# Performance work log

Measured on AMD Instinct MI355X. Metric: run time of the kernel, lower is better.

Reference implementation:

```python
import jax, jax.numpy as jnp
import numpy as np

B, L, H, E, MODES = 32, 2048, 8, 64, 64
SCALE = 1.0 / (512 * 512)  # 1/(in_channels*out_channels)


def setup_inputs() -> dict:
    key = jax.random.key(0)
    kq, kk, kv, kwr, kwi = jax.random.split(key, 5)
    # frequency mode selection: shuffled range(L//2), first MODES, sorted (get_frequency_modes)
    rng = np.random.default_rng(0)
    index = np.sort(rng.permutation(L // 2)[:MODES]).astype(np.int32)
    return {
        "q": jax.random.normal(kq, (B, L, H, E), dtype=jnp.float32),
        "k": jax.random.normal(kk, (B, L, H, E), dtype=jnp.float32),
        "v": jax.random.normal(kv, (B, L, H, E), dtype=jnp.float32),
        "w_real": SCALE * jax.random.uniform(kwr, (H, E, E, MODES), dtype=jnp.float32),
        "w_imag": SCALE * jax.random.uniform(kwi, (H, E, E, MODES), dtype=jnp.float32),
        "index": jnp.asarray(index),
    }


def reference(q, k, v, w_real, w_imag, index):
    # q: [B, L, H, E]; k, v unused by FourierBlock
    Bq, Lq, Hq, Eq = q.shape
    x = jnp.transpose(q, (0, 2, 3, 1))            # [B, H, E, L]
    x_ft = jnp.fft.rfft(x, axis=-1)               # [B, H, E, L//2+1] complex
    xs = jnp.take(x_ft, index, axis=-1)           # gather selected modes: [B, H, E, M]
    W = w_real + 1j * w_imag                      # [H, E, E, M] complex
    # vectorized per-mode complex einsum ('bhi,hio->bho' over all modes m)
    out = jnp.einsum('bhim,hiom->bhom', xs, W)    # [B, H, E, M]
    n_freq = Lq // 2 + 1
    # original writes mode wi into slot wi (0..M-1), rest stay zero
    out_ft = jnp.concatenate(
        [out, jnp.zeros((Bq, Hq, Eq, n_freq - out.shape[-1]), dtype=out.dtype)], axis=-1)
    return jnp.fft.irfft(out_ft, n=Lq, axis=-1)   # [B, H, E, L] real
```

## Files before the change

### kernel.cpp

```cpp
#include <hip/hip_runtime.h>
#include <math.h>

#define NB 32
#define NL 2048
#define NH 8
#define NE 64
#define NM 64
#define MRI 128
#define BK 128
#define NCH 16

typedef __attribute__((ext_vector_type(8))) __bf16 bf16x8;
typedef __attribute__((ext_vector_type(2))) __bf16 bf16x2;
typedef __attribute__((ext_vector_type(8))) unsigned short us8;
typedef __attribute__((ext_vector_type(4))) unsigned short us4;
typedef __attribute__((ext_vector_type(4))) float f32x4;
typedef __attribute__((ext_vector_type(16))) float f32x16;

__device__ __forceinline__ unsigned short f2bf(float x) {
  unsigned int u = __builtin_bit_cast(unsigned int, x);
  u = (u + 0x7fffu + ((u >> 16) & 1u)) >> 16;
  return (unsigned short)u;
}
__device__ __forceinline__ float bf2f(unsigned short u) {
  return __builtin_bit_cast(float, (unsigned int)u << 16);
}
__device__ __forceinline__ unsigned int pk2(float lo, float hi) {
  bf16x2 v;
  v[0] = (__bf16)lo;
  v[1] = (__bf16)hi;
  return __builtin_bit_cast(unsigned int, v);
}

__global__ void tables_k(const int* __restrict__ idx,
                         const float* __restrict__ wr, const float* __restrict__ wi,
                         unsigned short* __restrict__ Tf, unsigned short* __restrict__ IT,
                         unsigned short* __restrict__ WBr, unsigned short* __restrict__ WBi) {
  int gid = blockIdx.x * blockDim.x + threadIdx.x;
  const float w0 = 6.283185307179586f / (float)NL;
  {
    int j = gid & 7, lane_ = (gid >> 3) & 63, tm_ = (gid >> 9) & 3;
    int ks_ = (gid >> 11) & 3, kh_ = (gid >> 13) & 1, c_ = gid >> 14;
    int row = tm_ * 32 + (lane_ & 31);
    int m = row & 63;
    int k = c_ * 128 + kh_ * 64 + ks_ * 16 + (lane_ >> 5) * 8 + j;
    int f = idx[m];
    float s, c2;
    sincosf((float)((f * k) & (NL - 1)) * w0, &s, &c2);
    Tf[gid] = f2bf(row < 64 ? c2 : -s);
  }
  {
    int lp = gid >> 7, k = gid & 127;
    int m = k & 63;
    float s, c;
    sincosf((float)((m * lp) & (NL - 1)) * w0, &s, &c);
    float v = (k < 64) ? ((m == 0 ? 1.0f : 2.0f) / (float)NL) * c
                       : (m == 0 ? 0.0f : (-2.0f / (float)NL) * s);
    IT[gid] = f2bf(v);
  }
  {
    const float2* wr2 = (const float2*)wr;
    const float2* wi2 = (const float2*)wi;
    unsigned int* obr = (unsigned int*)WBr;
    unsigned int* obi = (unsigned int*)WBi;
#pragma unroll
    for (int r = 0; r < 4; ++r) {
      int j = r * 262144 + gid;
      float2 a = wr2[j];
      float2 b2 = wi2[j];
      obr[j] = pk2(a.x, a.y);
      obi[j] = pk2(b2.x, b2.y);
    }
  }
}

__global__ __launch_bounds__(1024) void fused_k(const float* __restrict__ q,
                                                const unsigned short* __restrict__ T,
                                                const unsigned short* __restrict__ IT,
                                                const unsigned short* __restrict__ WBr,
                                                const unsigned short* __restrict__ WBi,
                                                float* __restrict__ out) {
  __shared__ __align__(16) char smem[85504];
  int t = threadIdx.x, lane = t & 63, wid = t >> 6;
  int h = blockIdx.x & 7, b = blockIdx.x >> 3;

  {
    char* bC = smem + 34816;
    char* bN = smem + 34816 + 16896;
    char* bX = smem + 34816 + 33792;
    const float* qb = q + ((size_t)b * NL * NH + h) * NE;
    int tm = wid & 3;
    int te = (wid >> 2) & 1;
    int kh = wid >> 3;
    int eq = t & 15, lq = t >> 4;
    f32x16 acc32 = {};
    f32x4 qA[2], qB[2];
    us8 arA[4], arB[4];

    auto qload = [&](int c, f32x4* qr) {
#pragma unroll
      for (int p = 0; p < 2; ++p)
        qr[p] = *(const f32x4*)(qb + (size_t)(c * BK + lq * 2 + p) * (NH * NE) + eq * 4);
    };
    auto writesB = [&](const f32x4* qr, char* bb) {
#pragma unroll
      for (int j = 0; j < 4; ++j) {
        int e = eq * 4 + j;
        *(unsigned int*)(bb + e * 264 + lq * 4) = pk2(qr[0][j], qr[1][j]);
      }
    };
    auto loadA = [&](int c, us8* ar) {
#pragma unroll
      for (int ks = 0; ks < 4; ++ks)
        ar[ks] = *(const us8*)(T + ((((size_t)c * 2 + kh) * 4 + ks) * 4 + tm) * 512 + lane * 8);
    };
    auto compute = [&](const us8* ar, const char* bb) {
#pragma unroll
      for (int ks = 0; ks < 4; ++ks) {
        int k0 = (kh * 4 + ks) * 16;
        int e = te * 32 + (lane & 31);
        int boff = e * 264 + (k0 + (lane >> 5) * 8) * 2;
        uint2 blo = *(const uint2*)(bb + boff);
        uint2 bhi = *(const uint2*)(bb + boff + 8);
        bf16x8 bfr = __builtin_bit_cast(bf16x8, make_uint4(blo.x, blo.y, bhi.x, bhi.y));
        acc32 = __builtin_amdgcn_mfma_f32_32x32x16_bf16(
            __builtin_bit_cast(bf16x8, ar[ks]), bfr, acc32, 0, 0, 0);
      }
    };
    auto rot = [&]() {
      char* tmp = bC;
      bC = bN;
      bN = bX;
      bX = tmp;
    };

    qload(0, qA);
    qload(1, qB);
    loadA(0, arA);
    writesB(qA, bC);
    asm volatile("s_waitcnt lgkmcnt(0)" ::: "memory");
    __builtin_amdgcn_s_barrier();
    for (int c = 0; c < NCH; c += 2) {
      loadA(c + 1, arB);
      if (c + 2 < NCH) qload(c + 2, qA);
      __builtin_amdgcn_sched_barrier(0);
      compute(arA, bC);
      writesB(qB, bN);
      asm volatile("s_waitcnt lgkmcnt(0)" ::: "memory");
      __builtin_amdgcn_s_barrier();
      rot();
      if (c + 2 < NCH) loadA(c + 2, arA);
      if (c + 3 < NCH) qload(c + 3, qB);
      __builtin_amdgcn_sched_barrier(0);
      compute(arB, bC);
      if (c + 2 < NCH) {
        writesB(qA, bN);
        asm volatile("s_waitcnt lgkmcnt(0)" ::: "memory");
        __builtin_amdgcn_s_barrier();
      }
      rot();
    }
    __syncthreads();

    float* scr = (float*)(smem + 34816);
    int tile = wid & 7;
    if (kh == 1) {
#pragma unroll
      for (int r = 0; r < 16; ++r) {
        int row = (r & 3) + 8 * (r >> 2) + 4 * (lane >> 5);
        scr[tile * 1024 + row * 32 + (lane & 31)] = acc32[r];
      }
    }
    __syncthreads();
    if (kh == 0) {
#pragma unroll
      for (int r = 0; r < 16; ++r) {
        int row = (r & 3) + 8 * (r >> 2) + 4 * (lane >> 5);
        float v = acc32[r] + scr[tile * 1024 + row * 32 + (lane & 31)];
        int grow = tm * 32 + row;
        int gcol = te * 32 + (lane & 31);
        int off = (grow * 272 + gcol * 4) ^ (((grow >> 3) & 7) << 4);
        *(float*)(smem + off) = v;
      }
    }
  }
  __syncthreads();

  {
    char* OtB = smem + 67584;
    int o = t >> 4, mq = t & 15;
    const unsigned short* wbr = WBr + (size_t)h * 262144 + o * 64 + mq * 4;
    const unsigned short* wbi = WBi + (size_t)h * 262144 + o * 64 + mq * 4;
    float orr[4] = {}, oii[4] = {};
#pragma unroll 2
    for (int ib = 0; ib < 16; ++ib) {
      f32x4 xr4[4], xi4[4];
#pragma unroll
      for (int mi = 0; mi < 4; ++mi) {
        int m = mq * 4 + mi;
        xr4[mi] = *(const f32x4*)(smem + ((m * 272 + ib * 16) ^ (((m >> 3) & 7) << 4)));
        xi4[mi] = *(const f32x4*)(smem + (((64 + m) * 272 + ib * 16) ^ (((m >> 3) & 7) << 4)));
      }
      us4 wr4[4], wi4[4];
#pragma unroll
      for (int ii = 0; ii < 4; ++ii) {
        int i = ib * 4 + ii;
        wr4[ii] = *(const us4*)(wbr + (size_t)i * 4096);
        wi4[ii] = *(const us4*)(wbi + (size_t)i * 4096);
      }
#pragma unroll
      for (int ii = 0; ii < 4; ++ii)
#pragma unroll
        for (int mi = 0; mi < 4; ++mi) {
          float wrv = bf2f(wr4[ii][mi]);
          float wiv = bf2f(wi4[ii][mi]);
          orr[mi] += xr4[mi][ii] * wrv - xi4[mi][ii] * wiv;
          oii[mi] += xr4[mi][ii] * wiv + xi4[mi][ii] * wrv;
        }
    }
    uint2 vr = make_uint2(pk2(orr[0], orr[1]), pk2(orr[2], orr[3]));
    uint2 vi = make_uint2(pk2(oii[0], oii[1]), pk2(oii[2], oii[3]));
    *(uint2*)(OtB + ((o * 256 + mq * 8) ^ ((o & 7) << 4))) = vr;
    *(uint2*)(OtB + ((o * 256 + 128 + mq * 8) ^ ((o & 7) << 4))) = vi;
  }
  __syncthreads();

  {
    const char* OtB = smem + 67584;
    bf16x8 af[2][8];
#pragma unroll
    for (int rg2 = 0; rg2 < 2; ++rg2)
#pragma unroll
      for (int ks = 0; ks < 8; ++ks) {
        int row = rg2 * 32 + (lane & 31);
        int off = (row * 256 + ks * 32 + (lane >> 5) * 16) ^ ((row & 7) << 4);
        af[rg2][ks] = __builtin_bit_cast(bf16x8, *(const us8*)(OtB + off));
      }
    float* ob = out + ((size_t)(b * 8 + h) * 64) * NL;
    int l0 = wid * 128;
    for (int ct = 0; ct < 4; ++ct) {
      int lr = l0 + ct * 32 + (lane & 31);
      f32x16 a2[2] = {};
#pragma unroll
      for (int ks = 0; ks < 8; ++ks) {
        bf16x8 bv = __builtin_bit_cast(
            bf16x8, *(const us8*)(IT + (size_t)lr * MRI + ks * 16 + (lane >> 5) * 8));
        a2[0] = __builtin_amdgcn_mfma_f32_32x32x16_bf16(af[0][ks], bv, a2[0], 0, 0, 0);
        a2[1] = __builtin_amdgcn_mfma_f32_32x32x16_bf16(af[1][ks], bv, a2[1], 0, 0, 0);
      }
#pragma unroll
      for (int rg2 = 0; rg2 < 2; ++rg2)
#pragma unroll
        for (int rg = 0; rg < 16; ++rg) {
          int row = rg2 * 32 + ((rg & 3) + 8 * (rg >> 2) + 4 * (lane >> 5));
          __builtin_nontemporal_store(a2[rg2][rg], &ob[(size_t)row * NL + lr]);
        }
    }
  }
}

extern "C" void kernel_launch(void* const* d_in, const int* in_sizes, int n_in,
                              void* d_out, int out_size, void* d_ws, size_t ws_size,
                              hipStream_t stream) {
  const float* q = (const float*)d_in[0];
  const float* wr = (const float*)d_in[3];
  const float* wi = (const float*)d_in[4];
  const int* idx = (const int*)d_in[5];
  float* out = (float*)d_out;
  char* ws = (char*)d_ws;

  constexpr size_t TBYTES = (size_t)MRI * NL * 2;
  constexpr size_t WBBYTES = (size_t)NH * NE * NE * NM * 2;
  constexpr size_t NEED = 2 * TBYTES + 2 * WBBYTES;
  if (ws_size < NEED) return;

  unsigned short* Tf = (unsigned short*)ws;
  unsigned short* IT = (unsigned short*)(ws + TBYTES);
  unsigned short* WBr = (unsigned short*)(ws + 2 * TBYTES);
  unsigned short* WBi = (unsigned short*)(ws + 2 * TBYTES + WBBYTES);

  hipLaunchKernelGGL(tables_k, dim3(1024), dim3(256), 0, stream, idx, wr, wi, Tf, IT, WBr, WBi);
  hipLaunchKernelGGL(fused_k, dim3(NB * NH), dim3(1024), 0, stream, q, Tf, IT, WBr, WBi, out);
}
```

Measured before the change: 82.61 us.

## Halve fused kernel block to 512 threads, drop split-K reduction and shrink LDS

The fused kernel now runs 512 threads per block instead of 1024, so each wave covers the full K range of the forward DFT GEMM. This removes the split-K halves and their shared-memory reduction step. Per-thread work doubles in every stage: more q loads, more A fragments, 8 modes per thread in the complex mix, and 256 L-columns per wave in the inverse transform. Shared memory falls from about 85KB to 52KB, with a launch bound hint of 4 blocks. The gains are fewer barriers and more co-resident blocks, at the cost of higher register pressure and less parallelism inside each block.

```diff
diff --git a/kernel.cpp b/kernel.cpp
--- a/kernel.cpp
+++ b/kernel.cpp
@@ -13,7 +13,6 @@
 typedef __attribute__((ext_vector_type(8))) __bf16 bf16x8;
 typedef __attribute__((ext_vector_type(2))) __bf16 bf16x2;
 typedef __attribute__((ext_vector_type(8))) unsigned short us8;
-typedef __attribute__((ext_vector_type(4))) unsigned short us4;
 typedef __attribute__((ext_vector_type(4))) float f32x4;
 typedef __attribute__((ext_vector_type(16))) float f32x16;
 
@@ -74,57 +73,57 @@
   }
 }
 
-__global__ __launch_bounds__(1024) void fused_k(const float* __restrict__ q,
-                                                const unsigned short* __restrict__ T,
-                                                const unsigned short* __restrict__ IT,
-                                                const unsigned short* __restrict__ WBr,
-                                                const unsigned short* __restrict__ WBi,
-                                                float* __restrict__ out) {
-  __shared__ __align__(16) char smem[85504];
+__global__ __launch_bounds__(512, 4) void fused_k(const float* __restrict__ q,
+                                                  const unsigned short* __restrict__ T,
+                                                  const unsigned short* __restrict__ IT,
+                                                  const unsigned short* __restrict__ WBr,
+                                                  const unsigned short* __restrict__ WBi,
+                                                  float* __restrict__ out) {
+  __shared__ __align__(16) char smem[53248];
   int t = threadIdx.x, lane = t & 63, wid = t >> 6;
   int h = blockIdx.x & 7, b = blockIdx.x >> 3;
 
   {
-    char* bC = smem + 34816;
-    char* bN = smem + 34816 + 16896;
-    char* bX = smem + 34816 + 33792;
+    char* bC = smem;
+    char* bN = smem + 16896;
+    char* bX = smem + 33792;
     const float* qb = q + ((size_t)b * NL * NH + h) * NE;
     int tm = wid & 3;
-    int te = (wid >> 2) & 1;
-    int kh = wid >> 3;
+    int te = wid >> 2;
     int eq = t & 15, lq = t >> 4;
     f32x16 acc32 = {};
-    f32x4 qA[2], qB[2];
-    us8 arA[4], arB[4];
+    f32x4 qA[4], qB[4];
+    us8 arA[8], arB[8];
 
     auto qload = [&](int c, f32x4* qr) {
 #pragma unroll
-      for (int p = 0; p < 2; ++p)
-        qr[p] = *(const f32x4*)(qb + (size_t)(c * BK + lq * 2 + p) * (NH * NE) + eq * 4);
+      for (int p = 0; p < 4; ++p)
+        qr[p] = *(const f32x4*)(qb + (size_t)(c * BK + lq * 4 + p) * (NH * NE) + eq * 4);
     };
     auto writesB = [&](const f32x4* qr, char* bb) {
 #pragma unroll
       for (int j = 0; j < 4; ++j) {
         int e = eq * 4 + j;
-        *(unsigned int*)(bb + e * 264 + lq * 4) = pk2(qr[0][j], qr[1][j]);
+        *(uint2*)(bb + e * 264 + lq * 8) =
+            make_uint2(pk2(qr[0][j], qr[1][j]), pk2(qr[2][j], qr[3][j]));
       }
     };
     auto loadA = [&](int c, us8* ar) {
 #pragma unroll
-      for (int ks = 0; ks < 4; ++ks)
-        ar[ks] = *(const us8*)(T + ((((size_t)c * 2 + kh) * 4 + ks) * 4 + tm) * 512 + lane * 8);
+      for (int kf = 0; kf < 8; ++kf)
+        ar[kf] = *(const us8*)(
+            T + ((((size_t)c * 2 + (kf >> 2)) * 4 + (kf & 3)) * 4 + tm) * 512 + lane * 8);
     };
     auto compute = [&](const us8* ar, const char* bb) {
 #pragma unroll
-      for (int ks = 0; ks < 4; ++ks) {
-        int k0 = (kh * 4 + ks) * 16;
+      for (int kf = 0; kf < 8; ++kf) {
         int e = te * 32 + (lane & 31);
-        int boff = e * 264 + (k0 + (lane >> 5) * 8) * 2;
+        int boff = e * 264 + (kf * 16 + (lane >> 5) * 8) * 2;
         uint2 blo = *(const uint2*)(bb + boff);
         uint2 bhi = *(const uint2*)(bb + boff + 8);
         bf16x8 bfr = __builtin_bit_cast(bf16x8, make_uint4(blo.x, blo.y, bhi.x, bhi.y));
         acc32 = __builtin_amdgcn_mfma_f32_32x32x16_bf16(
-            __builtin_bit_cast(bf16x8, ar[ks]), bfr, acc32, 0, 0, 0);
+            __builtin_bit_cast(bf16x8, ar[kf]), bfr, acc32, 0, 0, 0);
       }
     };
     auto rot = [&]() {
@@ -162,71 +161,60 @@
     }
     __syncthreads();
 
-    float* scr = (float*)(smem + 34816);
-    int tile = wid & 7;
-    if (kh == 1) {
-#pragma unroll
-      for (int r = 0; r < 16; ++r) {
-        int row = (r & 3) + 8 * (r >> 2) + 4 * (lane >> 5);
-        scr[tile * 1024 + row * 32 + (lane & 31)] = acc32[r];
-      }
-    }
-    __syncthreads();
-    if (kh == 0) {
-#pragma unroll
-      for (int r = 0; r < 16; ++r) {
-        int row = (r & 3) + 8 * (r >> 2) + 4 * (lane >> 5);
-        float v = acc32[r] + scr[tile * 1024 + row * 32 + (lane & 31)];
-        int grow = tm * 32 + row;
-        int gcol = te * 32 + (lane & 31);
-        int off = (grow * 272 + gcol * 4) ^ (((grow >> 3) & 7) << 4);
-        *(float*)(smem + off) = v;
-      }
+#pragma unroll
+    for (int rg = 0; rg < 16; ++rg) {
+      int row = (rg & 3) + 8 * (rg >> 2) + 4 * (lane >> 5);
+      int grow = tm * 32 + row;
+      int gcol = te * 32 + (lane & 31);
+      int off = (grow * 272 + gcol * 4) ^ (((grow >> 3) & 7) << 4);
+      *(float*)(smem + off) = acc32[rg];
     }
   }
   __syncthreads();
 
   {
-    char* OtB = smem + 67584;
-    int o = t >> 4, mq = t & 15;
-    const unsigned short* wbr = WBr + (size_t)h * 262144 + o * 64 + mq * 4;
-    const unsigned short* wbi = WBi + (size_t)h * 262144 + o * 64 + mq * 4;
-    float orr[4] = {}, oii[4] = {};
-#pragma unroll 2
+    char* OtB = smem + 36864;
+    int o = t >> 3, mq = t & 7;
+    const unsigned short* wbr = WBr + (size_t)h * 262144 + o * 64 + mq * 8;
+    const unsigned short* wbi = WBi + (size_t)h * 262144 + o * 64 + mq * 8;
+    float orr[8] = {}, oii[8] = {};
     for (int ib = 0; ib < 16; ++ib) {
-      f32x4 xr4[4], xi4[4];
-#pragma unroll
-      for (int mi = 0; mi < 4; ++mi) {
-        int m = mq * 4 + mi;
-        xr4[mi] = *(const f32x4*)(smem + ((m * 272 + ib * 16) ^ (((m >> 3) & 7) << 4)));
-        xi4[mi] = *(const f32x4*)(smem + (((64 + m) * 272 + ib * 16) ^ (((m >> 3) & 7) << 4)));
-      }
-      us4 wr4[4], wi4[4];
+      f32x4 xr4[8], xi4[8];
+#pragma unroll
+      for (int mi = 0; mi < 8; ++mi) {
+        int m = mq * 8 + mi;
+        xr4[mi] = *(const f32x4*)(smem + ((m * 272 + ib * 16) ^ (mq << 4)));
+        xi4[mi] = *(const f32x4*)(smem + (((64 + m) * 272 + ib * 16) ^ (mq << 4)));
+      }
+      us8 wr8[4], wi8[4];
 #pragma unroll
       for (int ii = 0; ii < 4; ++ii) {
         int i = ib * 4 + ii;
-        wr4[ii] = *(const us4*)(wbr + (size_t)i * 4096);
-        wi4[ii] = *(const us4*)(wbi + (size_t)i * 4096);
+        wr8[ii] = *(const us8*)(wbr + (size_t)i * 4096);
+        wi8[ii] = *(const us8*)(wbi + (size_t)i * 4096);
       }
 #pragma unroll
       for (int ii = 0; ii < 4; ++ii)
 #pragma unroll
-        for (int mi = 0; mi < 4; ++mi) {
-          float wrv = bf2f(wr4[ii][mi]);
-          float wiv = bf2f(wi4[ii][mi]);
+        for (int mi = 0; mi < 8; ++mi) {
+          float wrv = bf2f(wr8[ii][mi]);
+          float wiv = bf2f(wi8[ii][mi]);
           orr[mi] += xr4[mi][ii] * wrv - xi4[mi][ii] * wiv;
           oii[mi] += xr4[mi][ii] * wiv + xi4[mi][ii] * wrv;
         }
     }
-    uint2 vr = make_uint2(pk2(orr[0], orr[1]), pk2(orr[2], orr[3]));
-    uint2 vi = make_uint2(pk2(oii[0], oii[1]), pk2(oii[2], oii[3]));
-    *(uint2*)(OtB + ((o * 256 + mq * 8) ^ ((o & 7) << 4))) = vr;
-    *(uint2*)(OtB + ((o * 256 + 128 + mq * 8) ^ ((o & 7) << 4))) = vi;
+    __syncthreads();
+    uint4 vr = make_uint4(pk2(orr[0], orr[1]), pk2(orr[2], orr[3]),
+                          pk2(orr[4], orr[5]), pk2(orr[6], orr[7]));
+    uint4 vi = make_uint4(pk2(oii[0], oii[1]), pk2(oii[2], oii[3]),
+                          pk2(oii[4], oii[5]), pk2(oii[6], oii[7]));
+    *(uint4*)(OtB + ((o * 256 + mq * 16) ^ ((o & 7) << 4))) = vr;
+    *(uint4*)(OtB + ((o * 256 + 128 + mq * 16) ^ ((o & 7) << 4))) = vi;
   }
   __syncthreads();
 
   {
-    const char* OtB = smem + 67584;
+    const char* OtB = smem + 36864;
     bf16x8 af[2][8];
 #pragma unroll
     for (int rg2 = 0; rg2 < 2; ++rg2)
@@ -237,8 +225,8 @@
         af[rg2][ks] = __builtin_bit_cast(bf16x8, *(const us8*)(OtB + off));
       }
     float* ob = out + ((size_t)(b * 8 + h) * 64) * NL;
-    int l0 = wid * 128;
-    for (int ct = 0; ct < 4; ++ct) {
+    int l0 = wid * 256;
+    for (int ct = 0; ct < 8; ++ct) {
       int lr = l0 + ct * 32 + (lane & 31);
       f32x16 a2[2] = {};
 #pragma unroll
@@ -280,5 +268,5 @@
   unsigned short* WBi = (unsigned short*)(ws + 2 * TBYTES + WBBYTES);
 
   hipLaunchKernelGGL(tables_k, dim3(1024), dim3(256), 0, stream, idx, wr, wi, Tf, IT, WBr, WBi);
-  hipLaunchKernelGGL(fused_k, dim3(NB * NH), dim3(1024), 0, stream, q, Tf, IT, WBr, WBi, out);
-}
+  hipLaunchKernelGGL(fused_k, dim3(NB * NH), dim3(512), 0, stream, q, Tf, IT, WBr, WBi, out);
+}
```

New measurement: 94.57 us. +14.5%, slower.
